# Performance work log

Hardware: AMD Instinct MI355X
Metric: run time of the kernel (lower is better)

Reference implementation:

```python
import jax, jax.numpy as jnp
import numpy as np

NSIDE = 128
NPIX = 12 * NSIDE * NSIDE  # 196608
B, C_IN, C_OUT = 8, 16, 32


def setup_inputs() -> dict:
    key = jax.random.key(0)
    k1, k2, k3 = jax.random.split(key, 3)
    x = jax.random.normal(k1, (B, C_IN, NPIX), dtype=jnp.float32)
    # kaiming-normal-like init for Conv1d weight [out, in, 9]
    fan_in = C_IN * 9
    weight = jax.random.normal(k2, (C_OUT, C_IN, 9), dtype=jnp.float32) * jnp.sqrt(2.0 / fan_in)
    b = jnp.zeros((C_OUT,), dtype=jnp.float32)
    # neighbour indices in [0, NPIX]; value NPIX selects the zero-pad column
    neighbours = jax.random.randint(k3, (9 * NPIX,), 0, NPIX + 1, dtype=jnp.int32)
    return {"x": x, "weight": weight, "b": b, "neighbours": neighbours}


def reference(x, weight, b, neighbours):
    # F.pad(x, (0,1)) -> append one zero pixel column so index NPIX reads 0
    x_pad = jnp.pad(x, ((0, 0), (0, 0), (0, 1)))  # [B, C_in, NPIX+1]
    neigh = neighbours.reshape(NPIX, 9)
    # gather: [B, C_in, NPIX, 9]
    vec = x_pad[:, :, neigh]
    # Conv1d(kernel=9, stride=9) over flattened [B,C,9*NPIX] == per-pixel 9-tap contraction
    out = jnp.einsum('bcpk,ock->bop', vec, weight)  # [B, C_out, NPIX]
    return out + b[None, :, None]
```

## Files before the change

kernel.cpp:

```cpp
#include <hip/hip_runtime.h>
#include <hip/hip_bf16.h>

#define NSIDE 128
#define NPIX (12 * NSIDE * NSIDE)
#define BB 8
#define CIN 16
#define COUT 32
#define NROW (NPIX + 1)

typedef _Float16 half8 __attribute__((ext_vector_type(8)));
typedef float floatx16 __attribute__((ext_vector_type(16)));

__global__ __launch_bounds__(256) void prep_xt(const float* __restrict__ x,
                                               _Float16* __restrict__ xt) {
    int r = blockIdx.x * 256 + threadIdx.x;
    const int total = BB * NROW;
    if (r >= total) return;
    int b = r / NROW;
    int p = r - b * NROW;
    half8 lo, hi;
    if (p < NPIX) {
        const float* xp = x + (long)b * CIN * NPIX + p;
#pragma unroll
        for (int c = 0; c < 8; c++) lo[c] = (_Float16)xp[(long)c * NPIX];
#pragma unroll
        for (int c = 0; c < 8; c++) hi[c] = (_Float16)xp[(long)(c + 8) * NPIX];
    } else {
#pragma unroll
        for (int c = 0; c < 8; c++) { lo[c] = (_Float16)0.f; hi[c] = (_Float16)0.f; }
    }
    *(half8*)(xt + (long)r * 16)     = lo;
    *(half8*)(xt + (long)r * 16 + 8) = hi;
}

__global__ __launch_bounds__(256) void prep_wf(const float* __restrict__ w,
                                               _Float16* __restrict__ wf) {
    for (int e = threadIdx.x; e < 9 * 64 * 8; e += 256) {
        int k    = e >> 9;
        int lane = (e >> 3) & 63;
        int j    = e & 7;
        int o    = lane & 31;
        int c    = ((lane >> 5) << 3) + j;
        wf[e] = (_Float16)w[(o * CIN + c) * 9 + k];
    }
}

__global__ __launch_bounds__(256) void conv_main(const _Float16* __restrict__ xt,
                                                 const _Float16* __restrict__ wf,
                                                 const float* __restrict__ bias,
                                                 const int* __restrict__ nb,
                                                 float* __restrict__ out) {
    const int lane  = threadIdx.x & 63;
    const int wv    = threadIdx.x >> 6;
    const int tile  = blockIdx.x * 4 + wv;
    const int b     = tile / (NPIX / 32);
    const int pt    = tile - b * (NPIX / 32);
    const int p     = pt * 32 + (lane & 31);
    const int chalf = (lane >> 5) * 8;

    half8 wfrag[9];
#pragma unroll
    for (int k = 0; k < 9; k++)
        wfrag[k] = *(const half8*)(wf + ((k * 64 + lane) << 3));

    const int* nbp = nb + p * 9;
    int idx[9];
#pragma unroll
    for (int k = 0; k < 9; k++) idx[k] = nbp[k];

    const _Float16* xb = xt + (long)b * NROW * 16 + chalf;
    floatx16 acc;
#pragma unroll
    for (int i = 0; i < 16; i++) acc[i] = 0.f;

#pragma unroll
    for (int k = 0; k < 9; k++) {
        half8 v = *(const half8*)(xb + (long)idx[k] * 16);
        acc = __builtin_amdgcn_mfma_f32_32x32x16_f16(wfrag[k], v, acc, 0, 0, 0);
    }

    float* outb = out + ((long)b * COUT) * NPIX + p;
#pragma unroll
    for (int r = 0; r < 16; r++) {
        int o = (r & 3) + ((r >> 2) << 3) + ((lane >> 5) << 2);
        outb[(long)o * NPIX] = acc[r] + bias[o];
    }
}

extern "C" void kernel_launch(void* const* d_in, const int* in_sizes, int n_in,
                              void* d_out, int out_size, void* d_ws, size_t ws_size,
                              hipStream_t stream) {
    const float* x    = (const float*)d_in[0];
    const float* w    = (const float*)d_in[1];
    const float* bias = (const float*)d_in[2];
    const int*   nb   = (const int*)d_in[3];
    float*       out  = (float*)d_out;

    _Float16* wf = (_Float16*)d_ws;
    _Float16* xt = (_Float16*)((char*)d_ws + 16384);

    int rows = BB * NROW;
    hipLaunchKernelGGL(prep_xt, dim3((rows + 255) / 256), dim3(256), 0, stream, x, xt);
    hipLaunchKernelGGL(prep_wf, dim3(1), dim3(256), 0, stream, w, wf);
    hipLaunchKernelGGL(conv_main, dim3(BB * NPIX / 32 / 4), dim3(256), 0, stream,
                       xt, wf, bias, nb, out);
}
```

Measured before the change: 410.3 us.

## Vectorize fp16 transpose prep and process two pixel tiles per wave

The transpose kernel now has each thread load four pixels across all 16 channels with float4 reads and write them with nontemporal stores. The zero pad row moves into the weight-prep kernel. The main kernel gives each wave two 32-pixel tiles and issues all gathers before the MFMAs, to expose more memory-level parallelism and reuse the weight fragments. Output stores and neighbour-index loads become nontemporal. The cost is higher register use, which may lower occupancy.

After: 519.5 us. 26.6% more time.

```diff
diff --git a/kernel.cpp b/kernel.cpp
--- a/kernel.cpp
+++ b/kernel.cpp
@@ -13,28 +13,35 @@
 
 __global__ __launch_bounds__(256) void prep_xt(const float* __restrict__ x,
                                                _Float16* __restrict__ xt) {
-    int r = blockIdx.x * 256 + threadIdx.x;
-    const int total = BB * NROW;
-    if (r >= total) return;
-    int b = r / NROW;
-    int p = r - b * NROW;
-    half8 lo, hi;
-    if (p < NPIX) {
-        const float* xp = x + (long)b * CIN * NPIX + p;
+    int t = blockIdx.x * 256 + threadIdx.x;
+    const int P4 = NPIX / 4;
+    int b  = t / P4;
+    int p4 = t - b * P4;
+    const float* xb = x + (long)b * CIN * NPIX + p4 * 4;
+    float4 ld[16];
 #pragma unroll
-        for (int c = 0; c < 8; c++) lo[c] = (_Float16)xp[(long)c * NPIX];
+    for (int c = 0; c < 16; c++)
+        ld[c] = *(const float4*)(xb + (long)c * NPIX);
+    _Float16* dst = xt + ((long)b * NROW + p4 * 4) * 16;
 #pragma unroll
-        for (int c = 0; c < 8; c++) hi[c] = (_Float16)xp[(long)(c + 8) * NPIX];
-    } else {
-#pragma unroll
-        for (int c = 0; c < 8; c++) { lo[c] = (_Float16)0.f; hi[c] = (_Float16)0.f; }
+    for (int i = 0; i < 4; i++) {
+        half8 lo, hi;
+        lo[0]=(_Float16)(&ld[0].x)[i];  lo[1]=(_Float16)(&ld[1].x)[i];
+        lo[2]=(_Float16)(&ld[2].x)[i];  lo[3]=(_Float16)(&ld[3].x)[i];
+        lo[4]=(_Float16)(&ld[4].x)[i];  lo[5]=(_Float16)(&ld[5].x)[i];
+        lo[6]=(_Float16)(&ld[6].x)[i];  lo[7]=(_Float16)(&ld[7].x)[i];
+        hi[0]=(_Float16)(&ld[8].x)[i];  hi[1]=(_Float16)(&ld[9].x)[i];
+        hi[2]=(_Float16)(&ld[10].x)[i]; hi[3]=(_Float16)(&ld[11].x)[i];
+        hi[4]=(_Float16)(&ld[12].x)[i]; hi[5]=(_Float16)(&ld[13].x)[i];
+        hi[6]=(_Float16)(&ld[14].x)[i]; hi[7]=(_Float16)(&ld[15].x)[i];
+        __builtin_nontemporal_store(lo, (half8*)(dst + i * 16));
+        __builtin_nontemporal_store(hi, (half8*)(dst + i * 16 + 8));
     }
-    *(half8*)(xt + (long)r * 16)     = lo;
-    *(half8*)(xt + (long)r * 16 + 8) = hi;
 }
 
 __global__ __launch_bounds__(256) void prep_wf(const float* __restrict__ w,
-                                               _Float16* __restrict__ wf) {
+                                               _Float16* __restrict__ wf,
+                                               _Float16* __restrict__ xt) {
     for (int e = threadIdx.x; e < 9 * 64 * 8; e += 256) {
         int k    = e >> 9;
         int lane = (e >> 3) & 63;
@@ -42,6 +49,11 @@
         int o    = lane & 31;
         int c    = ((lane >> 5) << 3) + j;
         wf[e] = (_Float16)w[(o * CIN + c) * 9 + k];
+    }
+    int t = threadIdx.x;
+    if (t < 128) {
+        int b = t >> 4, c = t & 15;
+        xt[((long)b * NROW + NPIX) * 16 + c] = (_Float16)0.f;
     }
 }
 
@@ -52,10 +64,11 @@
                                                  float* __restrict__ out) {
     const int lane  = threadIdx.x & 63;
     const int wv    = threadIdx.x >> 6;
-    const int tile  = blockIdx.x * 4 + wv;
-    const int b     = tile / (NPIX / 32);
-    const int pt    = tile - b * (NPIX / 32);
-    const int p     = pt * 32 + (lane & 31);
+    const int pair  = blockIdx.x * 4 + wv;
+    const int PPB   = NPIX / 64;
+    const int b     = pair / PPB;
+    const int p0    = (pair - b * PPB) * 64 + (lane & 31);
+    const int p1    = p0 + 32;
     const int chalf = (lane >> 5) * 8;
 
     half8 wfrag[9];
@@ -63,27 +76,37 @@
     for (int k = 0; k < 9; k++)
         wfrag[k] = *(const half8*)(wf + ((k * 64 + lane) << 3));
 
-    const int* nbp = nb + p * 9;
-    int idx[9];
+    int idx0[9], idx1[9];
+    const int* nbp0 = nb + p0 * 9;
+    const int* nbp1 = nb + p1 * 9;
 #pragma unroll
-    for (int k = 0; k < 9; k++) idx[k] = nbp[k];
+    for (int k = 0; k < 9; k++) idx0[k] = __builtin_nontemporal_load(nbp0 + k);
+#pragma unroll
+    for (int k = 0; k < 9; k++) idx1[k] = __builtin_nontemporal_load(nbp1 + k);
 
     const _Float16* xb = xt + (long)b * NROW * 16 + chalf;
-    floatx16 acc;
+    half8 v0[9], v1[9];
 #pragma unroll
-    for (int i = 0; i < 16; i++) acc[i] = 0.f;
+    for (int k = 0; k < 9; k++) v0[k] = *(const half8*)(xb + (long)idx0[k] * 16);
+#pragma unroll
+    for (int k = 0; k < 9; k++) v1[k] = *(const half8*)(xb + (long)idx1[k] * 16);
 
+    floatx16 acc0, acc1;
+#pragma unroll
+    for (int i = 0; i < 16; i++) { acc0[i] = 0.f; acc1[i] = 0.f; }
 #pragma unroll
     for (int k = 0; k < 9; k++) {
-        half8 v = *(const half8*)(xb + (long)idx[k] * 16);
-        acc = __builtin_amdgcn_mfma_f32_32x32x16_f16(wfrag[k], v, acc, 0, 0, 0);
+        acc0 = __builtin_amdgcn_mfma_f32_32x32x16_f16(wfrag[k], v0[k], acc0, 0, 0, 0);
+        acc1 = __builtin_amdgcn_mfma_f32_32x32x16_f16(wfrag[k], v1[k], acc1, 0, 0, 0);
     }
 
-    float* outb = out + ((long)b * COUT) * NPIX + p;
+    float* outb = out + (long)b * COUT * NPIX;
 #pragma unroll
     for (int r = 0; r < 16; r++) {
         int o = (r & 3) + ((r >> 2) << 3) + ((lane >> 5) << 2);
-        outb[(long)o * NPIX] = acc[r] + bias[o];
+        float bv = bias[o];
+        __builtin_nontemporal_store(acc0[r] + bv, outb + (long)o * NPIX + p0);
+        __builtin_nontemporal_store(acc1[r] + bv, outb + (long)o * NPIX + p1);
     }
 }
 
@@ -99,9 +122,8 @@
     _Float16* wf = (_Float16*)d_ws;
     _Float16* xt = (_Float16*)((char*)d_ws + 16384);
 
-    int rows = BB * NROW;
-    hipLaunchKernelGGL(prep_xt, dim3((rows + 255) / 256), dim3(256), 0, stream, x, xt);
-    hipLaunchKernelGGL(prep_wf, dim3(1), dim3(256), 0, stream, w, wf);
-    hipLaunchKernelGGL(conv_main, dim3(BB * NPIX / 32 / 4), dim3(256), 0, stream,
+    hipLaunchKernelGGL(prep_xt, dim3(BB * NPIX / 4 / 256), dim3(256), 0, stream, x, xt);
+    hipLaunchKernelGGL(prep_wf, dim3(1), dim3(256), 0, stream, w, wf, xt);
+    hipLaunchKernelGGL(conv_main, dim3(BB * NPIX / 64 / 4), dim3(256), 0, stream,
                        xt, wf, bias, nb, out);
 }
```
